# Performance work log

Hardware: AMD Instinct MI355X
Metric: run time of the kernel (lower is better)

The kernel has to match this reference:

```python
import jax, jax.numpy as jnp
import numpy as np

S, H, NH, DS = 4096, 1024, 2, 64   # seq_len, hidden, num_heads, static_in_size
HD = H // NH                        # head_dim = 512
EPS = 1e-5                          # eqx.nn.LayerNorm default eps


def setup_inputs() -> dict:
    key = jax.random.key(0)
    ks = jax.random.split(key, 11)
    sc = lambda n: 1.0 / np.sqrt(n)
    return {
        "inputs": jax.random.normal(ks[0], (S, H), jnp.float32),
        "static_data": jax.random.normal(ks[1], (DS,), jnp.float32),
        "base_mask": jax.random.randint(ks[2], (S,), 0, 2).astype(bool),
        "Wq": jax.random.normal(ks[3], (H, H), jnp.float32) * sc(H),
        "Wk": jax.random.normal(ks[4], (H, H), jnp.float32) * sc(H),
        "Wv": jax.random.normal(ks[5], (H, H), jnp.float32) * sc(H),
        "Wo": jax.random.normal(ks[6], (H, H), jnp.float32) * sc(H),
        "Ws": jax.random.normal(ks[7], (H, DS), jnp.float32) * sc(DS),
        "bs": jax.random.normal(ks[8], (H,), jnp.float32) * 0.01,
        "ln_w": jnp.ones((H,), jnp.float32),
        "ln_b": jnp.zeros((H,), jnp.float32),
    }


def reference(inputs, static_data, base_mask, Wq, Wk, Wv, Wo, Ws, bs, ln_w, ln_b):
    # static embedding injected into keys/values
    semb = Ws @ static_data + bs                      # [H]
    kv_in = inputs + semb[None, :]                    # [S, H]

    # per-head projections (eqx Linear: y = W @ x, no bias in MHA projections)
    q = (inputs @ Wq.T).reshape(S, NH, HD)
    k = (kv_in @ Wk.T).reshape(S, NH, HD)
    v = (kv_in @ Wv.T).reshape(S, NH, HD)

    logits = jnp.einsum('qhd,khd->hqk', q, k) / np.sqrt(HD)  # [NH, S, S]

    # head 0: irregular mask (base_mask broadcast over queries); head 1: all-ones
    irregular = jnp.broadcast_to(base_mask[None, :], (S, S))
    mask = jnp.stack([irregular, jnp.ones((S, S), bool)], axis=0)  # [2, S, S]
    logits = jnp.where(mask, logits, jnp.finfo(logits.dtype).min)

    attn = jax.nn.softmax(logits, axis=-1)
    ctx = jnp.einsum('hqk,khd->qhd', attn, v).reshape(S, H)
    out = ctx @ Wo.T                                  # output projection

    # dropout_rate = 0 -> identity; residual + per-token LayerNorm
    res = out + inputs
    mu = res.mean(-1, keepdims=True)
    var = res.var(-1, keepdims=True)
    return (res - mu) / jnp.sqrt(var + EPS) * ln_w + ln_b
```

## Files before the change

kernel.cpp:

```cpp
#include <hip/hip_runtime.h>
#include <stdint.h>

#define S_LEN  4096
#define HID    1024
#define NHEAD  2
#define HDIM   512
#define NSPLIT 4
#define KS_STRIDE 520
#define LN_EPS 1e-5f

typedef __bf16 bf16x8 __attribute__((ext_vector_type(8)));
typedef float  f32x4  __attribute__((ext_vector_type(4)));

__device__ __forceinline__ float b2f(unsigned short u) {
    return __uint_as_float(((unsigned int)u) << 16);
}
__device__ __forceinline__ unsigned short f2b(float f) {
    unsigned int u = __float_as_uint(f);
    u += 0x7FFFu + ((u >> 16) & 1u);
    return (unsigned short)(u >> 16);
}

__device__ __forceinline__ void async_cp16(const void* g, void* l) {
    __builtin_amdgcn_global_load_lds(
        (const __attribute__((address_space(1))) unsigned int*)g,
        (__attribute__((address_space(3))) unsigned int*)l, 16, 0, 0);
}

__global__ void k_cvt4s(const float* __restrict__ i0, const float* __restrict__ i1,
                        const float* __restrict__ i2, const float* __restrict__ i3,
                        unsigned short* __restrict__ o0, unsigned short* __restrict__ o1,
                        unsigned short* __restrict__ o2, unsigned short* __restrict__ o3,
                        const float* __restrict__ Ws, const float* __restrict__ sd,
                        const float* __restrict__ bs, float* __restrict__ semb) {
    int z = blockIdx.y;
    if (z == 4) {
        int j = blockIdx.x * blockDim.x + threadIdx.x;
        if (j >= HID) return;
        float acc = bs[j];
        const float* row = Ws + j * 64;
        #pragma unroll
        for (int d = 0; d < 64; ++d) acc += row[d] * sd[d];
        semb[j] = acc;
        return;
    }
    const float* in = z == 0 ? i0 : z == 1 ? i1 : z == 2 ? i2 : i3;
    unsigned short* o = z == 0 ? o0 : z == 1 ? o1 : z == 2 ? o2 : o3;
    int i = (blockIdx.x * blockDim.x + threadIdx.x) * 8;
    float4 a = *(const float4*)(in + i);
    float4 b = *(const float4*)(in + i + 4);
    unsigned short r[8] = {f2b(a.x), f2b(a.y), f2b(a.z), f2b(a.w),
                           f2b(b.x), f2b(b.y), f2b(b.z), f2b(b.w)};
    *(uint4*)(o + i) = *(const uint4*)r;
}

__global__ void k_kvin(const float* __restrict__ X,
                       const float* __restrict__ semb,
                       unsigned short* __restrict__ Xb,
                       unsigned short* __restrict__ kv) {
    int idx = (blockIdx.x * blockDim.x + threadIdx.x) * 8;
    if (idx >= S_LEN * HID) return;
    int col = idx & (HID - 1);
    float4 a = *(const float4*)(X + idx);
    float4 b = *(const float4*)(X + idx + 4);
    unsigned short xo[8] = {f2b(a.x), f2b(a.y), f2b(a.z), f2b(a.w),
                            f2b(b.x), f2b(b.y), f2b(b.z), f2b(b.w)};
    *(uint4*)(Xb + idx) = *(const uint4*)xo;
    unsigned short o[8];
    o[0] = f2b(a.x + semb[col + 0]);
    o[1] = f2b(a.y + semb[col + 1]);
    o[2] = f2b(a.z + semb[col + 2]);
    o[3] = f2b(a.w + semb[col + 3]);
    o[4] = f2b(b.x + semb[col + 4]);
    o[5] = f2b(b.y + semb[col + 5]);
    o[6] = f2b(b.z + semb[col + 6]);
    o[7] = f2b(b.w + semb[col + 7]);
    *(uint4*)(kv + idx) = *(const uint4*)o;
}

__device__ __forceinline__
void gemm128(const unsigned short* __restrict__ A,
             const unsigned short* __restrict__ B,
             unsigned short* __restrict__ Cb,
             int nx, int ldc) {
    __shared__ unsigned short As[128 * 32];
    __shared__ unsigned short Bs[128 * 32];
    int tid  = threadIdx.x;
    int wave = tid >> 6, lane = tid & 63;
    int quad = lane >> 4, l16 = lane & 15;
    int wm = wave >> 1, wn = wave & 1;
    int m0 = (blockIdx.x / nx) * 128, n0 = (blockIdx.x % nx) * 128;

    f32x4 zero = {0.f, 0.f, 0.f, 0.f};
    f32x4 acc[4][4];
    #pragma unroll
    for (int i = 0; i < 4; ++i)
        #pragma unroll
        for (int j = 0; j < 4; ++j) acc[i][j] = zero;

    for (int k0 = 0; k0 < HID; k0 += 32) {
        #pragma unroll
        for (int i = 0; i < 2; ++i) {
            int c = tid + i * 256;
            async_cp16(A + (m0 + (c >> 2)) * HID + k0 + (c & 3) * 8, As + c * 8);
            async_cp16(B + (n0 + (c >> 2)) * HID + k0 + (c & 3) * 8, Bs + c * 8);
        }
        __syncthreads();
        bf16x8 af[4], bfr[4];
        #pragma unroll
        for (int i = 0; i < 4; ++i)
            af[i] = *(const bf16x8*)(As + (wm * 64 + i * 16 + l16) * 32 + quad * 8);
        #pragma unroll
        for (int j = 0; j < 4; ++j)
            bfr[j] = *(const bf16x8*)(Bs + (wn * 64 + j * 16 + l16) * 32 + quad * 8);
        #pragma unroll
        for (int i = 0; i < 4; ++i)
            #pragma unroll
            for (int j = 0; j < 4; ++j)
                acc[i][j] = __builtin_amdgcn_mfma_f32_16x16x32_bf16(af[i], bfr[j], acc[i][j], 0, 0, 0);
        __syncthreads();
    }

    #pragma unroll
    for (int i = 0; i < 4; ++i) {
        int rbase = m0 + wm * 64 + i * 16 + quad * 4;
        #pragma unroll
        for (int j = 0; j < 4; ++j) {
            int col = n0 + wn * 64 + j * 16 + l16;
            #pragma unroll
            for (int r = 0; r < 4; ++r)
                Cb[(size_t)(rbase + r) * ldc + col] = f2b(acc[i][j][r]);
        }
    }
}

__global__ __launch_bounds__(256)
void k_gemm_qkv(const unsigned short* __restrict__ Xb,
                const unsigned short* __restrict__ kvin,
                const unsigned short* __restrict__ Wqb,
                const unsigned short* __restrict__ Wkb,
                const unsigned short* __restrict__ Wvb,
                unsigned short* __restrict__ Qb,
                unsigned short* __restrict__ Kb,
                unsigned short* __restrict__ Vt) {
    int z = blockIdx.z;
    if (z == 0)      gemm128(Xb,   Wqb,  Qb,  8, HID);
    else if (z == 1) gemm128(kvin, Wkb,  Kb,  8, HID);
    else             gemm128(Wvb,  kvin, Vt, 32, S_LEN);
}

__global__ __launch_bounds__(256)
void k_gemm_o(const unsigned short* __restrict__ A,
              const unsigned short* __restrict__ B,
              float* __restrict__ Cf,
              const float* __restrict__ Xres) {
    __shared__ unsigned short As[64 * 32];
    __shared__ unsigned short Bs[128 * 32];
    int tid  = threadIdx.x;
    int wave = tid >> 6, lane = tid & 63;
    int quad = lane >> 4, l16 = lane & 15;
    int m0 = (blockIdx.x >> 3) * 64, n0 = (blockIdx.x & 7) * 128;

    f32x4 zero = {0.f, 0.f, 0.f, 0.f};
    f32x4 acc[4][2];
    #pragma unroll
    for (int i = 0; i < 4; ++i)
        #pragma unroll
        for (int j = 0; j < 2; ++j) acc[i][j] = zero;

    for (int k0 = 0; k0 < HID; k0 += 32) {
        async_cp16(A + (m0 + (tid >> 2)) * HID + k0 + (tid & 3) * 8, As + tid * 8);
        #pragma unroll
        for (int i = 0; i < 2; ++i) {
            int c = tid + i * 256;
            async_cp16(B + (n0 + (c >> 2)) * HID + k0 + (c & 3) * 8, Bs + c * 8);
        }
        __syncthreads();
        bf16x8 af[4], bfr[2];
        #pragma unroll
        for (int i = 0; i < 4; ++i)
            af[i] = *(const bf16x8*)(As + (i * 16 + l16) * 32 + quad * 8);
        #pragma unroll
        for (int j = 0; j < 2; ++j)
            bfr[j] = *(const bf16x8*)(Bs + (wave * 32 + j * 16 + l16) * 32 + quad * 8);
        #pragma unroll
        for (int i = 0; i < 4; ++i)
            #pragma unroll
            for (int j = 0; j < 2; ++j)
                acc[i][j] = __builtin_amdgcn_mfma_f32_16x16x32_bf16(af[i], bfr[j], acc[i][j], 0, 0, 0);
        __syncthreads();
    }

    #pragma unroll
    for (int i = 0; i < 4; ++i) {
        int rbase = m0 + i * 16 + quad * 4;
        #pragma unroll
        for (int j = 0; j < 2; ++j) {
            int col = n0 + wave * 32 + j * 16 + l16;
            #pragma unroll
            for (int r = 0; r < 4; ++r) {
                size_t o = (size_t)(rbase + r) * HID + col;
                Cf[o] = acc[i][j][r] + Xres[o];
            }
        }
    }
}

__global__ __launch_bounds__(512, 2)
void k_flash(const unsigned short* __restrict__ Q,
             const unsigned short* __restrict__ K,
             const unsigned short* __restrict__ Vt,
             const int* __restrict__ mask,
             unsigned short* __restrict__ Opart,
             float* __restrict__ Lbuf) {
    __shared__ unsigned short Ks[2][32 * KS_STRIDE];
    __shared__ __bf16 Ps[2][128][40];
    int tid  = threadIdx.x;
    int wave = tid >> 6, lane = tid & 63;
    int quad = lane >> 4, l16 = lane & 15;
    int head = blockIdx.x / NSPLIT, split = blockIdx.x % NSPLIT, qtile = blockIdx.y;

    int qrow = qtile * 128 + wave * 16 + l16;
    const unsigned short* qp = Q + qrow * HID + head * HDIM;
    bf16x8 qf[16];
    #pragma unroll
    for (int t = 0; t < 16; ++t) qf[t] = *(const bf16x8*)(qp + t * 32 + quad * 8);

    float lsum[4];
    #pragma unroll
    for (int r = 0; r < 4; ++r) lsum[r] = 0.f;
    f32x4 zero = {0.f, 0.f, 0.f, 0.f};
    f32x4 oacc[8][4];
    #pragma unroll
    for (int mt = 0; mt < 8; ++mt)
        #pragma unroll
        for (int nt = 0; nt < 4; ++nt) oacc[mt][nt] = zero;

    const float scale = 0.044194173824159216f;
    const unsigned short* Kbase = K + head * HDIM;
    const unsigned short* vptr = Vt + (size_t)(head * HDIM + wave * 64 + l16) * S_LEN
                                    + split * 1024 + quad * 8;

    auto stageK = [&](int kt, int buf) {
        int kb = split * 1024 + kt * 32;
        #pragma unroll
        for (int i = 0; i < 4; ++i) {
            int c = tid + i * 512;
            int row = c >> 6, col = (c & 63) * 8;
            async_cp16(Kbase + (kb + row) * HID + col, &Ks[buf][row * KS_STRIDE + col]);
        }
    };

    stageK(0, 0);
    int mk0 = 1, mk1 = 1;
    if (head == 0) {
        mk0 = mask[split * 1024 + l16];
        mk1 = mask[split * 1024 + 16 + l16];
    }

    bf16x8 vf[4];
    for (int it = 0; it < 32; ++it) {
        int cur = it & 1;
        __syncthreads();

        if (it < 31) stageK(it + 1, cur ^ 1);

        __builtin_amdgcn_s_setprio(1);
        if (it > 0) {
            #pragma unroll
            for (int mt = 0; mt < 8; ++mt) {
                bf16x8 pf = *(const bf16x8*)&Ps[cur ^ 1][mt * 16 + l16][quad * 8];
                #pragma unroll
                for (int nt = 0; nt < 4; ++nt)
                    oacc[mt][nt] = __builtin_amdgcn_mfma_f32_16x16x32_bf16(pf, vf[nt], oacc[mt][nt], 0, 0, 0);
            }
        }

        #pragma unroll
        for (int nt = 0; nt < 4; ++nt)
            vf[nt] = *(const bf16x8*)(vptr + (size_t)nt * 16 * S_LEN + it * 32);

        f32x4 sacc[2];
        sacc[0] = zero; sacc[1] = zero;
        #pragma unroll
        for (int nt = 0; nt < 2; ++nt)
            #pragma unroll
            for (int t = 0; t < 16; ++t) {
                bf16x8 kf = *(const bf16x8*)&Ks[cur][(nt * 16 + l16) * KS_STRIDE + t * 32 + quad * 8];
                sacc[nt] = __builtin_amdgcn_mfma_f32_16x16x32_bf16(qf[t], kf, sacc[nt], 0, 0, 0);
            }
        __builtin_amdgcn_s_setprio(0);

        bool keep0 = mk0 != 0;
        bool keep1 = mk1 != 0;
        #pragma unroll
        for (int r = 0; r < 4; ++r) {
            float p0 = keep0 ? __expf(fminf(sacc[0][r] * scale, 30.f)) : 0.f;
            float p1 = keep1 ? __expf(fminf(sacc[1][r] * scale, 30.f)) : 0.f;
            lsum[r] += p0 + p1;
            Ps[cur][wave * 16 + quad * 4 + r][l16]      = (__bf16)p0;
            Ps[cur][wave * 16 + quad * 4 + r][16 + l16] = (__bf16)p1;
        }

        if (head == 0 && it < 31) {
            int kn = split * 1024 + (it + 1) * 32;
            mk0 = mask[kn + l16];
            mk1 = mask[kn + 16 + l16];
        }
    }

    __syncthreads();
    #pragma unroll
    for (int mt = 0; mt < 8; ++mt) {
        bf16x8 pf = *(const bf16x8*)&Ps[1][mt * 16 + l16][quad * 8];
        #pragma unroll
        for (int nt = 0; nt < 4; ++nt)
            oacc[mt][nt] = __builtin_amdgcn_mfma_f32_16x16x32_bf16(pf, vf[nt], oacc[mt][nt], 0, 0, 0);
    }

    #pragma unroll
    for (int r = 0; r < 4; ++r) {
        float s = lsum[r];
        #pragma unroll
        for (int off = 1; off < 16; off <<= 1)
            s += __shfl_xor(s, off, 64);
        lsum[r] = s;
    }
    int lrow = qtile * 128 + wave * 16 + quad * 4;
    if (l16 == 0) {
        #pragma unroll
        for (int r = 0; r < 4; ++r)
            Lbuf[(split * NHEAD + head) * S_LEN + lrow + r] = lsum[r];
    }
    unsigned short* op = Opart + (size_t)split * S_LEN * HID;
    #pragma unroll
    for (int mt = 0; mt < 8; ++mt)
        #pragma unroll
        for (int nt = 0; nt < 4; ++nt)
            #pragma unroll
            for (int r = 0; r < 4; ++r)
                op[(qtile * 128 + mt * 16 + quad * 4 + r) * HID +
                   head * HDIM + wave * 64 + nt * 16 + l16] = f2b(oacc[mt][nt][r]);
}

__global__ void k_combine(const unsigned short* __restrict__ Opart,
                          const float* __restrict__ Lbuf,
                          unsigned short* __restrict__ ctx) {
    const int SH = S_LEN * HID;
    int idx = blockIdx.x * blockDim.x + threadIdx.x;
    if (idx >= SH) return;
    int s = idx >> 10;
    int h = (idx >> 9) & 1;
    float l = 0.f, v = 0.f;
    #pragma unroll
    for (int z = 0; z < NSPLIT; ++z) {
        l += Lbuf[(z * NHEAD + h) * S_LEN + s];
        v += b2f(Opart[(size_t)z * SH + idx]);
    }
    ctx[idx] = f2b(v / l);
}

__global__ __launch_bounds__(256)
void k_ln(const float* __restrict__ res,
          const float* __restrict__ w,
          const float* __restrict__ b,
          float* __restrict__ out) {
    __shared__ float red[8];
    int s = blockIdx.x, tid = threadIdx.x;
    const float* row = res + s * HID;
    float x[4], s1 = 0.f, s2 = 0.f;
    #pragma unroll
    for (int i = 0; i < 4; ++i) {
        x[i] = row[tid + i * 256];
        s1 += x[i]; s2 += x[i] * x[i];
    }
    #pragma unroll
    for (int off = 1; off < 64; off <<= 1) {
        s1 += __shfl_xor(s1, off, 64);
        s2 += __shfl_xor(s2, off, 64);
    }
    int wave = tid >> 6;
    if ((tid & 63) == 0) { red[wave] = s1; red[4 + wave] = s2; }
    __syncthreads();
    s1 = red[0] + red[1] + red[2] + red[3];
    s2 = red[4] + red[5] + red[6] + red[7];
    float mu   = s1 * (1.f / HID);
    float var  = s2 * (1.f / HID) - mu * mu;
    float rstd = rsqrtf(var + LN_EPS);
    #pragma unroll
    for (int i = 0; i < 4; ++i) {
        int col = tid + i * 256;
        out[s * HID + col] = (x[i] - mu) * rstd * w[col] + b[col];
    }
}

extern "C" void kernel_launch(void* const* d_in, const int* in_sizes, int n_in,
                              void* d_out, int out_size, void* d_ws, size_t ws_size,
                              hipStream_t stream) {
    const float* X   = (const float*)d_in[0];
    const float* sd  = (const float*)d_in[1];
    const int*   msk = (const int*)d_in[2];
    const float* Wq  = (const float*)d_in[3];
    const float* Wk  = (const float*)d_in[4];
    const float* Wv  = (const float*)d_in[5];
    const float* Wo  = (const float*)d_in[6];
    const float* Wsp = (const float*)d_in[7];
    const float* bsp = (const float*)d_in[8];
    const float* lw  = (const float*)d_in[9];
    const float* lb  = (const float*)d_in[10];
    float* out = (float*)d_out;

    char* ws = (char*)d_ws;
    const size_t MB = 1ull << 20;
    float*          semb  = (float*)(ws);
    float*          Lbuf  = (float*)(ws + (1ull << 16));
    unsigned short* Xb    = (unsigned short*)(ws + 1 * MB);
    unsigned short* kvin  = (unsigned short*)(ws + 9 * MB);
    unsigned short* Qb    = (unsigned short*)(ws + 17 * MB);
    unsigned short* Kb    = (unsigned short*)(ws + 25 * MB);
    unsigned short* Vt    = (unsigned short*)(ws + 33 * MB);
    unsigned short* ctx   = (unsigned short*)(ws + 41 * MB);
    unsigned short* Wqb   = (unsigned short*)(ws + 49 * MB);
    unsigned short* Wkb   = (unsigned short*)(ws + 51 * MB);
    unsigned short* Wvb   = (unsigned short*)(ws + 53 * MB);
    unsigned short* Wob   = (unsigned short*)(ws + 55 * MB);
    float*          resf  = (float*)(ws + 17 * MB);
    unsigned short* Opart = (unsigned short*)(ws + 57 * MB);

    const int SH = S_LEN * HID;
    const int WW = HID * HID;

    k_cvt4s<<<dim3(WW / 8 / 256, 5), dim3(256), 0, stream>>>(
        Wq, Wk, Wv, Wo, Wqb, Wkb, Wvb, Wob, Wsp, sd, bsp, semb);

    k_kvin<<<dim3(SH / 8 / 256), dim3(256), 0, stream>>>(X, semb, Xb, kvin);

    k_gemm_qkv<<<dim3(256, 1, 3), dim3(256), 0, stream>>>(Xb, kvin, Wqb, Wkb, Wvb, Qb, Kb, Vt);

    k_flash<<<dim3(NHEAD * NSPLIT, S_LEN / 128), dim3(512), 0, stream>>>(
        Qb, Kb, Vt, msk, Opart, Lbuf);

    k_combine<<<dim3(SH / 256), dim3(256), 0, stream>>>(Opart, Lbuf, ctx);
    k_gemm_o<<<dim3(512), dim3(256), 0, stream>>>(ctx, Wob, resf, X);
    k_ln<<<dim3(S_LEN), dim3(256), 0, stream>>>(resf, lw, lb, out);
}
```

Before: 264.9 us.

## Fuse split-K combine into output GEMM and XOR-swizzle P tile in LDS

Removes the separate combine kernel. The output-projection GEMM now reads the four split partial outputs, sums them, scales by the inverse softmax denominator and writes bf16 into its A tile in LDS, so the ctx buffer round trip and one launch go away. The A-tile load becomes a synchronous global load with VALU work instead of an async copy, and the partials are re-read by each of the 8 column blocks. Separately, the flash kernel XOR-swizzles the column index of the P tile in LDS to reduce bank conflicts on its writes and reads.

Result: slower. 282.0 us (+6.5%).

```diff
diff --git a/kernel.cpp b/kernel.cpp
--- a/kernel.cpp
+++ b/kernel.cpp
@@ -150,17 +150,31 @@
 }
 
 __global__ __launch_bounds__(256)
-void k_gemm_o(const unsigned short* __restrict__ A,
+void k_gemm_o(const unsigned short* __restrict__ Opart,
+              const float* __restrict__ Lbuf,
               const unsigned short* __restrict__ B,
               float* __restrict__ Cf,
               const float* __restrict__ Xres) {
     __shared__ unsigned short As[64 * 32];
     __shared__ unsigned short Bs[128 * 32];
+    const size_t SH = (size_t)S_LEN * HID;
     int tid  = threadIdx.x;
     int wave = tid >> 6, lane = tid & 63;
     int quad = lane >> 4, l16 = lane & 15;
     int m0 = (blockIdx.x >> 3) * 64, n0 = (blockIdx.x & 7) * 128;
 
+    int arow  = m0 + (tid >> 2);
+    int acol8 = (tid & 3) * 8;
+    float rinv[NHEAD];
+    #pragma unroll
+    for (int h = 0; h < NHEAD; ++h) {
+        float l = 0.f;
+        #pragma unroll
+        for (int z = 0; z < NSPLIT; ++z)
+            l += Lbuf[(z * NHEAD + h) * S_LEN + arow];
+        rinv[h] = 1.f / l;
+    }
+
     f32x4 zero = {0.f, 0.f, 0.f, 0.f};
     f32x4 acc[4][2];
     #pragma unroll
@@ -169,11 +183,27 @@
         for (int j = 0; j < 2; ++j) acc[i][j] = zero;
 
     for (int k0 = 0; k0 < HID; k0 += 32) {
-        async_cp16(A + (m0 + (tid >> 2)) * HID + k0 + (tid & 3) * 8, As + tid * 8);
         #pragma unroll
         for (int i = 0; i < 2; ++i) {
             int c = tid + i * 256;
             async_cp16(B + (n0 + (c >> 2)) * HID + k0 + (c & 3) * 8, Bs + c * 8);
+        }
+        {
+            float rv = rinv[k0 >> 9];
+            const unsigned short* ap = Opart + (size_t)arow * HID + k0 + acol8;
+            float s[8] = {0.f, 0.f, 0.f, 0.f, 0.f, 0.f, 0.f, 0.f};
+            #pragma unroll
+            for (int z = 0; z < NSPLIT; ++z) {
+                uint4 v = *(const uint4*)(ap + z * SH);
+                unsigned short us[8];
+                *(uint4*)us = v;
+                #pragma unroll
+                for (int e = 0; e < 8; ++e) s[e] += b2f(us[e]);
+            }
+            unsigned short o8[8];
+            #pragma unroll
+            for (int e = 0; e < 8; ++e) o8[e] = f2b(s[e] * rv);
+            *(uint4*)(As + tid * 8) = *(const uint4*)o8;
         }
         __syncthreads();
         bf16x8 af[4], bfr[2];
@@ -241,6 +271,9 @@
     const unsigned short* vptr = Vt + (size_t)(head * HDIM + wave * 64 + l16) * S_LEN
                                     + split * 1024 + quad * 8;
 
+    const int wcx = (quad & 2) << 3;
+    const int rcx = (l16 & 8) << 1;
+
     auto stageK = [&](int kt, int buf) {
         int kb = split * 1024 + kt * 32;
         #pragma unroll
@@ -269,7 +302,7 @@
         if (it > 0) {
             #pragma unroll
             for (int mt = 0; mt < 8; ++mt) {
-                bf16x8 pf = *(const bf16x8*)&Ps[cur ^ 1][mt * 16 + l16][quad * 8];
+                bf16x8 pf = *(const bf16x8*)&Ps[cur ^ 1][mt * 16 + l16][(quad * 8) ^ rcx];
                 #pragma unroll
                 for (int nt = 0; nt < 4; ++nt)
                     oacc[mt][nt] = __builtin_amdgcn_mfma_f32_16x16x32_bf16(pf, vf[nt], oacc[mt][nt], 0, 0, 0);
@@ -298,8 +331,9 @@
             float p0 = keep0 ? __expf(fminf(sacc[0][r] * scale, 30.f)) : 0.f;
             float p1 = keep1 ? __expf(fminf(sacc[1][r] * scale, 30.f)) : 0.f;
             lsum[r] += p0 + p1;
-            Ps[cur][wave * 16 + quad * 4 + r][l16]      = (__bf16)p0;
-            Ps[cur][wave * 16 + quad * 4 + r][16 + l16] = (__bf16)p1;
+            int row = wave * 16 + quad * 4 + r;
+            Ps[cur][row][l16 ^ wcx]        = (__bf16)p0;
+            Ps[cur][row][(16 + l16) ^ wcx] = (__bf16)p1;
         }
 
         if (head == 0 && it < 31) {
@@ -312,7 +346,7 @@
     __syncthreads();
     #pragma unroll
     for (int mt = 0; mt < 8; ++mt) {
-        bf16x8 pf = *(const bf16x8*)&Ps[1][mt * 16 + l16][quad * 8];
+        bf16x8 pf = *(const bf16x8*)&Ps[1][mt * 16 + l16][(quad * 8) ^ rcx];
         #pragma unroll
         for (int nt = 0; nt < 4; ++nt)
             oacc[mt][nt] = __builtin_amdgcn_mfma_f32_16x16x32_bf16(pf, vf[nt], oacc[mt][nt], 0, 0, 0);
@@ -341,23 +375,6 @@
             for (int r = 0; r < 4; ++r)
                 op[(qtile * 128 + mt * 16 + quad * 4 + r) * HID +
                    head * HDIM + wave * 64 + nt * 16 + l16] = f2b(oacc[mt][nt][r]);
-}
-
-__global__ void k_combine(const unsigned short* __restrict__ Opart,
-                          const float* __restrict__ Lbuf,
-                          unsigned short* __restrict__ ctx) {
-    const int SH = S_LEN * HID;
-    int idx = blockIdx.x * blockDim.x + threadIdx.x;
-    if (idx >= SH) return;
-    int s = idx >> 10;
-    int h = (idx >> 9) & 1;
-    float l = 0.f, v = 0.f;
-    #pragma unroll
-    for (int z = 0; z < NSPLIT; ++z) {
-        l += Lbuf[(z * NHEAD + h) * S_LEN + s];
-        v += b2f(Opart[(size_t)z * SH + idx]);
-    }
-    ctx[idx] = f2b(v / l);
 }
 
 __global__ __launch_bounds__(256)
@@ -419,7 +436,6 @@
     unsigned short* Qb    = (unsigned short*)(ws + 17 * MB);
     unsigned short* Kb    = (unsigned short*)(ws + 25 * MB);
     unsigned short* Vt    = (unsigned short*)(ws + 33 * MB);
-    unsigned short* ctx   = (unsigned short*)(ws + 41 * MB);
     unsigned short* Wqb   = (unsigned short*)(ws + 49 * MB);
     unsigned short* Wkb   = (unsigned short*)(ws + 51 * MB);
     unsigned short* Wvb   = (unsigned short*)(ws + 53 * MB);
@@ -440,7 +456,6 @@
     k_flash<<<dim3(NHEAD * NSPLIT, S_LEN / 128), dim3(512), 0, stream>>>(
         Qb, Kb, Vt, msk, Opart, Lbuf);
 
-    k_combine<<<dim3(SH / 256), dim3(256), 0, stream>>>(Opart, Lbuf, ctx);
-    k_gemm_o<<<dim3(512), dim3(256), 0, stream>>>(ctx, Wob, resf, X);
+    k_gemm_o<<<dim3(512), dim3(256), 0, stream>>>(Opart, Lbuf, Wob, resf, X);
     k_ln<<<dim3(S_LEN), dim3(256), 0, stream>>>(resf, lw, lb, out);
 }
```
